# Kernel optimization log

Hardware: AMD Instinct MI355X
Metric: run time of the kernel (lower is better)

Reference implementation:

```python
import jax, jax.numpy as jnp
import numpy as np

B, S, E, NH = 2, 1024, 2048, 16
DH = E // NH
EPS = 1e-6

def setup_inputs() -> dict:
    key = jax.random.key(0)
    ks = jax.random.split(key, 6)
    q = jax.random.normal(ks[0], (B, S, E), dtype=jnp.float32)
    k = jax.random.normal(ks[1], (B, S, E), dtype=jnp.float32)
    v = jax.random.normal(ks[2], (B, S, E), dtype=jnp.float32)
    Wi = jax.random.normal(ks[3], (3 * E, NH), dtype=jnp.float32) * 0.02
    bi = jax.random.normal(ks[4], (NH,), dtype=jnp.float32) * 0.1
    Wf = jax.random.normal(ks[5], (3 * E, NH), dtype=jnp.float32) * 0.02
    bf = jnp.linspace(3.0, 6.0, NH, dtype=jnp.float32)  # bias_linspace_initializer(3,6)
    ln_scale = jnp.ones((E,), dtype=jnp.float32)
    return {"q": q, "k": k, "v": v, "Wi": Wi, "bi": bi, "Wf": Wf, "bf": bf, "ln_scale": ln_scale}

def _mlstm_forward(q, k, v, Wi, bi, Wf, bf, ln_scale):
    b, s, e = q.shape
    nh = Wi.shape[1]
    dh = e // nh
    x = jnp.concatenate([q, k, v], axis=-1)                     # (B,S,3E)
    ig = (x @ Wi + bi).transpose(0, 2, 1)[..., None]            # (B,NH,S,1)
    fg = (x @ Wf + bf).transpose(0, 2, 1)[..., None]            # (B,NH,S,1)
    split = lambda t: t.reshape(b, s, nh, dh).transpose(0, 2, 1, 3)
    qh, kh, vh = split(q), split(k), split(v)                   # (B,NH,S,DH)
    # parallel_stabilized_simple backend
    log_f = jax.nn.log_sigmoid(fg)                              # (B,NH,S,1)
    log_f_cum = jnp.concatenate(
        [jnp.zeros((b, nh, 1, 1), q.dtype), jnp.cumsum(log_f, axis=2)], axis=2
    )                                                           # (B,NH,S+1,1)
    # D[i,j] = cumsum[i] - cumsum[j] on causal part
    fg_mat = log_f_cum - jnp.transpose(log_f_cum, (0, 1, 3, 2)) # (B,NH,S+1,S+1)
    ltr = jnp.tril(jnp.ones((s, s), dtype=bool))
    log_fg = jnp.where(ltr, fg_mat[:, :, 1:, 1:], -jnp.inf)     # (B,NH,S,S)
    log_D = log_fg + jnp.transpose(ig, (0, 1, 3, 2))            # + i_j per column
    max_log_D = jnp.max(log_D, axis=-1, keepdims=True)          # (B,NH,S,1)
    D = jnp.exp(log_D - max_log_D)
    qk = jnp.einsum('bhsd,bhtd->bhst', qh, kh) / jnp.sqrt(jnp.asarray(dh, q.dtype))
    C = qk * D                                                  # (B,NH,S,S)
    normalizer = jnp.maximum(jnp.abs(C.sum(-1, keepdims=True)), jnp.exp(-max_log_D))
    Cn = C / (normalizer + EPS)
    h = jnp.einsum('bhst,bhtd->bhsd', Cn, vh)                   # (B,NH,S,DH)
    # MultiHeadLayerNorm: normalize over DH per head, scale (no bias)
    mu = h.mean(-1, keepdims=True)
    var = ((h - mu) ** 2).mean(-1, keepdims=True)
    hn = (h - mu) * jax.lax.rsqrt(var + EPS)
    hn = hn * ln_scale.reshape(1, nh, 1, dh)
    return hn.transpose(0, 2, 1, 3).reshape(b, s, e)            # (B,S,E)

def reference(q, k, v, Wi, bi, Wf, bf, ln_scale):
    return _mlstm_forward(q, k, v, Wi, bi, Wf, bf, ln_scale)
```

## Files before the change

kernel.cpp:

```cpp
#include <hip/hip_runtime.h>
#include <hip/hip_bf16.h>

#define B_   2
#define S_   1024
#define E_   2048
#define NH_  16
#define DH_  128
#define EPS_ 1e-6f

using half8   = __attribute__((ext_vector_type(8))) _Float16;
using floatx4 = __attribute__((ext_vector_type(4))) float;

__device__ __forceinline__ half8 cvt8h(const float* __restrict__ p) {
    float4 a = *(const float4*)p;
    float4 b = *(const float4*)(p + 4);
    half8 r;
    r[0] = (_Float16)a.x; r[1] = (_Float16)a.y;
    r[2] = (_Float16)a.z; r[3] = (_Float16)a.w;
    r[4] = (_Float16)b.x; r[5] = (_Float16)b.y;
    r[6] = (_Float16)b.z; r[7] = (_Float16)b.w;
    return r;
}

__global__ __launch_bounds__(256, 4) void gates_kernel(
    const float* __restrict__ q, const float* __restrict__ k,
    const float* __restrict__ v, const float* __restrict__ Wi,
    const float* __restrict__ Wf, float* __restrict__ pre_i,
    float* __restrict__ pre_f, _Float16* __restrict__ qhg,
    _Float16* __restrict__ khg, _Float16* __restrict__ vtg)
{
    __shared__ __attribute__((aligned(16))) _Float16 xs[32 * 264];
    __shared__ __attribute__((aligned(16))) _Float16 wt[32 * 264];

    const int t    = threadIdx.x;
    const int w    = t >> 6, lane = t & 63, quad = lane >> 4, l15 = lane & 15;
    const int mw   = w & 1, nw = w >> 1;
    const int m0   = blockIdx.x * 32;
    const int by   = blockIdx.y;
    const int kbase = by * 768;
    const int bblk = m0 >> 10;
    const int s0   = m0 & 1023;

    floatx4 acc = {0.f, 0.f, 0.f, 0.f};

    for (int c = 0; c < 3; ++c) {
        __syncthreads();
        const int e0   = kbase + c * 256;
        const int tsel = e0 >> 11;
        const int el0  = e0 & 2047;
        const float* xb = (tsel == 0) ? q : (tsel == 1) ? k : v;
        _Float16* fout = (tsel == 0) ? qhg : khg;
        #pragma unroll
        for (int i = 0; i < 4; ++i) {
            int g = t + i * 256;
            int row = g >> 5, grp = g & 31;
            half8 s8 = cvt8h(xb + (size_t)(m0 + row) * E_ + el0 + grp * 8);
            *(half8*)(&xs[row * 264 + grp * 8]) = s8;
            if (tsel < 2) {
                int el = el0 + grp * 8;
                int h  = el >> 7, d = el & 127;
                *(half8*)(fout + ((size_t)(bblk * NH_ + h) * S_ + s0 + row) * DH_ + d) = s8;
            }
        }
        {
            const int kk = t;
            const float* wiRow = Wi + (size_t)(e0 + kk) * NH_;
            const float* wfRow = Wf + (size_t)(e0 + kk) * NH_;
            float wif[16], wff[16];
            #pragma unroll
            for (int i4 = 0; i4 < 4; ++i4) {
                float4 a = *(const float4*)(wiRow + i4 * 4);
                wif[i4*4+0]=a.x; wif[i4*4+1]=a.y; wif[i4*4+2]=a.z; wif[i4*4+3]=a.w;
                float4 b = *(const float4*)(wfRow + i4 * 4);
                wff[i4*4+0]=b.x; wff[i4*4+1]=b.y; wff[i4*4+2]=b.z; wff[i4*4+3]=b.w;
            }
            #pragma unroll
            for (int hh = 0; hh < 16; ++hh) wt[hh * 264 + kk]        = (_Float16)wif[hh];
            #pragma unroll
            for (int hh = 0; hh < 16; ++hh) wt[(16 + hh) * 264 + kk] = (_Float16)wff[hh];
        }
        __syncthreads();
        if (tsel == 2) {
            const int col = t;
            const int el  = el0 + col;
            const int h   = el >> 7, d = el & 127;
            _Float16 tmp[32];
            #pragma unroll
            for (int r = 0; r < 32; ++r) tmp[r] = xs[r * 264 + col];
            const size_t vo = ((size_t)(bblk * NH_ + h) * DH_ + d) * S_ + s0;
            #pragma unroll
            for (int i = 0; i < 4; ++i)
                *(half8*)(vtg + vo + i * 8) = *(half8*)(&tmp[i * 8]);
        }
        #pragma unroll
        for (int ks = 0; ks < 8; ++ks) {
            half8 af = *(const half8*)(&xs[(mw * 16 + l15) * 264 + ks * 32 + quad * 8]);
            half8 bw = *(const half8*)(&wt[(nw * 16 + l15) * 264 + ks * 32 + quad * 8]);
            acc = __builtin_amdgcn_mfma_f32_16x16x32_f16(af, bw, acc, 0, 0, 0);
        }
    }
    #pragma unroll
    for (int reg = 0; reg < 4; ++reg) {
        int m   = m0 + mw * 16 + quad * 4 + reg;
        int b   = m >> 10, s = m & 1023;
        int col = nw * 16 + l15;
        float vacc = acc[reg];
        if (col < 16)
            pre_i[((size_t)(by * 32 + b * NH_ + col)) * S_ + s] = vacc;
        else
            pre_f[((size_t)(by * 32 + b * NH_ + col - 16)) * S_ + s] = vacc;
    }
}

__global__ __launch_bounds__(1024, 1) void scan_kernel(
    const float* __restrict__ pre_i, const float* __restrict__ pre_f,
    float* __restrict__ Aj, float* __restrict__ Cq,
    float* __restrict__ NFo, const float* __restrict__ bi,
    const float* __restrict__ bfb)
{
    __shared__ float wsumF[16], wmaxA[16];
    const int bh   = blockIdx.x;
    const int h    = bh & 15;
    const int t    = threadIdx.x;
    const int lane = t & 63, wv = t >> 6;

    float igv = bi[h], x = bfb[h];
    #pragma unroll
    for (int y = 0; y < 8; ++y) {
        igv += pre_i[((size_t)(y * 32 + bh)) * S_ + t];
        x   += pre_f[((size_t)(y * 32 + bh)) * S_ + t];
    }
    float lfv = (x >= 0.f) ? -log1pf(__expf(-x)) : (x - log1pf(__expf(x)));

    float sc = lfv;
    #pragma unroll
    for (int off = 1; off < 64; off <<= 1) {
        float o = __shfl_up(sc, off);
        if (lane >= off) sc += o;
    }
    if (lane == 63) wsumF[wv] = sc;
    __syncthreads();
    float Foff = 0.f;
    for (int i = 0; i < wv; ++i) Foff += wsumF[i];
    float F = Foff + sc;
    float a = igv - F;

    float ms = a;
    #pragma unroll
    for (int off = 1; off < 64; off <<= 1) {
        float o = __shfl_up(ms, off);
        if (lane >= off) ms = fmaxf(ms, o);
    }
    if (lane == 63) wmaxA[wv] = ms;
    __syncthreads();
    float Moff = -3.0e38f;
    for (int i = 0; i < wv; ++i) Moff = fmaxf(Moff, wmaxA[i]);
    float M = fmaxf(Moff, ms);

    size_t o = (size_t)bh * S_ + t;
    Aj[o]  = a;
    Cq[o]  = -M;
    NFo[o] = expf(fminf(-(F + M), 80.f));
}

__global__ __launch_bounds__(256, 2) void attn_kernel(
    const _Float16* __restrict__ qh, const _Float16* __restrict__ kh,
    const _Float16* __restrict__ vtg, const float* __restrict__ Aj,
    const float* __restrict__ Cq, const float* __restrict__ NFi,
    const float* __restrict__ lnsc, float* __restrict__ out)
{
    __shared__ __attribute__((aligned(16))) _Float16 Ks[64 * 136];
    __shared__ __attribute__((aligned(16))) _Float16 Vt[128 * 72];
    __shared__ __attribute__((aligned(16))) _Float16 Pb[64 * 72];
    __shared__ float aj[64];

    const int t    = threadIdx.x;
    const int w    = t >> 6, lane = t & 63, quad = lane >> 4, l15 = lane & 15;
    const int L    = blockIdx.x;
    int qi, bh;
    if (L < 256) { qi = L >> 5;                bh = L & 31; }
    else         { qi = 15 - ((L - 256) >> 5); bh = (L - 256) & 31; }
    const int b    = bh >> 4, h = bh & 15;
    const int q0   = qi * 64;
    const int krow = t >> 2, kd0 = (t & 3) * 32;
    const int vd   = t >> 1, vj0 = (t & 1) * 32;

    float ci_r[4], nfv_r[4];
    #pragma unroll
    for (int reg = 0; reg < 4; ++reg) {
        int rl = w * 16 + quad * 4 + reg;
        ci_r[reg]  = Cq[(size_t)bh * S_ + q0 + rl];
        nfv_r[reg] = NFi[(size_t)bh * S_ + q0 + rl];
    }
    half8 aq[4];
    {
        const _Float16* qrow = qh + ((size_t)bh * S_ + q0 + w * 16 + l15) * DH_;
        #pragma unroll
        for (int ks = 0; ks < 4; ++ks)
            aq[ks] = *(const half8*)(qrow + ks * 32 + quad * 8);
    }

    half8 kreg[4], vreg[4];
    float ajreg = 0.f;
    {
        const _Float16* kp = kh + ((size_t)bh * S_ + krow) * DH_ + kd0;
        const _Float16* vp = vtg + ((size_t)bh * DH_ + vd) * S_ + vj0;
        #pragma unroll
        for (int i = 0; i < 4; ++i) { kreg[i] = *(const half8*)(kp + i * 8);
                                      vreg[i] = *(const half8*)(vp + i * 8); }
    }
    if (t < 64) ajreg = Aj[(size_t)bh * S_ + t];

    #pragma unroll
    for (int i = 0; i < 4; ++i) {
        *(half8*)(&Ks[krow * 136 + kd0 + i * 8]) = kreg[i];
        *(half8*)(&Vt[vd * 72 + vj0 + i * 8])    = vreg[i];
    }
    if (t < 64) aj[t] = ajreg;
    __syncthreads();

    floatx4 acc_h[8];
    #pragma unroll
    for (int i = 0; i < 8; ++i) acc_h[i] = (floatx4){0.f, 0.f, 0.f, 0.f};
    float lrun[4] = {0.f, 0.f, 0.f, 0.f};
    const float rscale = 0.08838834764831845f;

    for (int kt = 0; kt <= qi; ++kt) {
        if (kt < qi) {
            const int j0n = (kt + 1) * 64;
            const _Float16* kp = kh + ((size_t)bh * S_ + j0n + krow) * DH_ + kd0;
            const _Float16* vp = vtg + ((size_t)bh * DH_ + vd) * S_ + j0n + vj0;
            #pragma unroll
            for (int i = 0; i < 4; ++i) { kreg[i] = *(const half8*)(kp + i * 8);
                                          vreg[i] = *(const half8*)(vp + i * 8); }
            if (t < 64) ajreg = Aj[(size_t)bh * S_ + j0n + t];
        }

        floatx4 sacc[4];
        #pragma unroll
        for (int nt = 0; nt < 4; ++nt) sacc[nt] = (floatx4){0.f, 0.f, 0.f, 0.f};
        #pragma unroll
        for (int ks = 0; ks < 4; ++ks) {
            #pragma unroll
            for (int nt = 0; nt < 4; ++nt) {
                half8 bk = *(const half8*)(&Ks[(nt * 16 + l15) * 136 + ks * 32 + quad * 8]);
                sacc[nt] = __builtin_amdgcn_mfma_f32_16x16x32_f16(aq[ks], bk, sacc[nt], 0, 0, 0);
            }
        }
        const bool diag = (kt == qi);
        #pragma unroll
        for (int nt = 0; nt < 4; ++nt) {
            int jl = nt * 16 + l15;
            float a_j = aj[jl];
            #pragma unroll
            for (int reg = 0; reg < 4; ++reg) {
                int rl = w * 16 + quad * 4 + reg;
                float p = 0.f;
                if (!diag || (jl <= rl))
                    p = sacc[nt][reg] * rscale * __expf(fminf(ci_r[reg] + a_j, 0.f));
                lrun[reg] += p;
                Pb[rl * 72 + jl] = (_Float16)p;
            }
        }
        #pragma unroll
        for (int ks2 = 0; ks2 < 2; ++ks2) {
            half8 ap = *(const half8*)(&Pb[(w * 16 + l15) * 72 + ks2 * 32 + quad * 8]);
            #pragma unroll
            for (int nt2 = 0; nt2 < 8; ++nt2) {
                half8 bv = *(const half8*)(&Vt[(nt2 * 16 + l15) * 72 + ks2 * 32 + quad * 8]);
                acc_h[nt2] = __builtin_amdgcn_mfma_f32_16x16x32_f16(ap, bv, acc_h[nt2], 0, 0, 0);
            }
        }

        __syncthreads();
        if (kt < qi) {
            #pragma unroll
            for (int i = 0; i < 4; ++i) {
                *(half8*)(&Ks[krow * 136 + kd0 + i * 8]) = kreg[i];
                *(half8*)(&Vt[vd * 72 + vj0 + i * 8])    = vreg[i];
            }
            if (t < 64) aj[t] = ajreg;
            __syncthreads();
        }
    }

    #pragma unroll
    for (int reg = 0; reg < 4; ++reg) {
        float l = lrun[reg];
        #pragma unroll
        for (int off = 1; off < 16; off <<= 1) l += __shfl_xor(l, off);
        int rl = w * 16 + quad * 4 + reg;
        float nrm = fmaxf(fabsf(l), nfv_r[reg]) + EPS_;
        float inv = 1.f / nrm;
        float hv[8];
        float sum = 0.f, sq = 0.f;
        #pragma unroll
        for (int nt2 = 0; nt2 < 8; ++nt2) {
            float x = acc_h[nt2][reg] * inv;
            hv[nt2] = x; sum += x; sq += x * x;
        }
        #pragma unroll
        for (int off = 1; off < 16; off <<= 1) {
            sum += __shfl_xor(sum, off);
            sq  += __shfl_xor(sq, off);
        }
        float mean = sum * (1.f / 128.f);
        float var  = fmaxf(sq * (1.f / 128.f) - mean * mean, 0.f);
        float rstd = rsqrtf(var + EPS_);
        size_t orow = ((size_t)b * S_ + q0 + rl) * E_ + h * DH_;
        #pragma unroll
        for (int nt2 = 0; nt2 < 8; ++nt2) {
            int d = nt2 * 16 + l15;
            out[orow + d] = (hv[nt2] - mean) * rstd * lnsc[h * DH_ + d];
        }
    }
}

extern "C" void kernel_launch(void* const* d_in, const int* in_sizes, int n_in,
                              void* d_out, int out_size, void* d_ws, size_t ws_size,
                              hipStream_t stream)
{
    const float* q    = (const float*)d_in[0];
    const float* k    = (const float*)d_in[1];
    const float* v    = (const float*)d_in[2];
    const float* Wi   = (const float*)d_in[3];
    const float* bi   = (const float*)d_in[4];
    const float* Wf   = (const float*)d_in[5];
    const float* bfb  = (const float*)d_in[6];
    const float* lnsc = (const float*)d_in[7];
    float* out        = (float*)d_out;

    const int NS  = B_ * NH_ * S_;
    float* pre_i = (float*)d_ws;
    float* pre_f = pre_i + 8 * NS;
    float* Aj    = pre_f + 8 * NS;
    float* Cq    = Aj + NS;
    float* NFa   = Cq + NS;
    _Float16* qh  = (_Float16*)(NFa + NS);
    _Float16* kh  = qh + (size_t)32 * S_ * DH_;
    _Float16* vtg = kh + (size_t)32 * S_ * DH_;

    gates_kernel<<<dim3(64, 8), 256, 0, stream>>>(q, k, v, Wi, Wf, pre_i, pre_f,
                                                  qh, kh, vtg);
    scan_kernel<<<dim3(32), 1024, 0, stream>>>(pre_i, pre_f, Aj, Cq, NFa, bi, bfb);
    attn_kernel<<<dim3(512), 256, 0, stream>>>(qh, kh, vtg, Aj, Cq, NFa, lnsc, out);
}
```

Measured before the change: 149.1 us.

## Pair complementary query tiles per block to balance causal work and share K/V tiles

Each block now handles two 64-row query tiles, qpi and 15-qpi. Waves 0-1 take the short tile and waves 2-3 the long one, with each wave computing 32 rows across two MFMA row-subtiles. K/V tiles are loaded once per block and reused by both query tiles, which gives every block the same causal work and halves the grid to 256 blocks. The cost is more registers per wave (launch bounds drop to one block per SM) and lower occupancy, and waves on the short tile sit idle through the later iterations while still hitting the barriers.

```diff
diff --git a/kernel.cpp b/kernel.cpp
--- a/kernel.cpp
+++ b/kernel.cpp
@@ -163,7 +163,7 @@
     NFo[o] = expf(fminf(-(F + M), 80.f));
 }
 
-__global__ __launch_bounds__(256, 2) void attn_kernel(
+__global__ __launch_bounds__(256, 1) void attn_kernel(
     const _Float16* __restrict__ qh, const _Float16* __restrict__ kh,
     const _Float16* __restrict__ vtg, const float* __restrict__ Aj,
     const float* __restrict__ Cq, const float* __restrict__ NFi,
@@ -171,33 +171,38 @@
 {
     __shared__ __attribute__((aligned(16))) _Float16 Ks[64 * 136];
     __shared__ __attribute__((aligned(16))) _Float16 Vt[128 * 72];
-    __shared__ __attribute__((aligned(16))) _Float16 Pb[64 * 72];
+    __shared__ __attribute__((aligned(16))) _Float16 Pb[128 * 72];
     __shared__ float aj[64];
 
     const int t    = threadIdx.x;
     const int w    = t >> 6, lane = t & 63, quad = lane >> 4, l15 = lane & 15;
-    const int L    = blockIdx.x;
-    int qi, bh;
-    if (L < 256) { qi = L >> 5;                bh = L & 31; }
-    else         { qi = 15 - ((L - 256) >> 5); bh = (L - 256) & 31; }
+    const int bid  = blockIdx.x;
+    const int bh   = bid & 31;
+    const int qpi  = bid >> 5;
     const int b    = bh >> 4, h = bh & 15;
-    const int q0   = qi * 64;
+    const int myq  = (w < 2) ? qpi : (15 - qpi);
+    const int ktN  = 15 - qpi;
+    const int qrow0 = myq * 64 + (w & 1) * 32;
+    const int prow0 = w * 32;
     const int krow = t >> 2, kd0 = (t & 3) * 32;
     const int vd   = t >> 1, vj0 = (t & 1) * 32;
 
-    float ci_r[4], nfv_r[4];
-    #pragma unroll
-    for (int reg = 0; reg < 4; ++reg) {
-        int rl = w * 16 + quad * 4 + reg;
-        ci_r[reg]  = Cq[(size_t)bh * S_ + q0 + rl];
-        nfv_r[reg] = NFi[(size_t)bh * S_ + q0 + rl];
-    }
-    half8 aq[4];
-    {
-        const _Float16* qrow = qh + ((size_t)bh * S_ + q0 + w * 16 + l15) * DH_;
+    float ci_r[2][4], nfv_r[2][4];
+    #pragma unroll
+    for (int s = 0; s < 2; ++s)
+        #pragma unroll
+        for (int reg = 0; reg < 4; ++reg) {
+            int rl = qrow0 + s * 16 + quad * 4 + reg;
+            ci_r[s][reg]  = Cq[(size_t)bh * S_ + rl];
+            nfv_r[s][reg] = NFi[(size_t)bh * S_ + rl];
+        }
+    half8 aq[2][4];
+    #pragma unroll
+    for (int s = 0; s < 2; ++s) {
+        const _Float16* qrow = qh + ((size_t)bh * S_ + qrow0 + s * 16 + l15) * DH_;
         #pragma unroll
         for (int ks = 0; ks < 4; ++ks)
-            aq[ks] = *(const half8*)(qrow + ks * 32 + quad * 8);
+            aq[s][ks] = *(const half8*)(qrow + ks * 32 + quad * 8);
     }
 
     half8 kreg[4], vreg[4];
@@ -219,14 +224,16 @@
     if (t < 64) aj[t] = ajreg;
     __syncthreads();
 
-    floatx4 acc_h[8];
-    #pragma unroll
-    for (int i = 0; i < 8; ++i) acc_h[i] = (floatx4){0.f, 0.f, 0.f, 0.f};
-    float lrun[4] = {0.f, 0.f, 0.f, 0.f};
+    floatx4 acc_h[2][8];
+    #pragma unroll
+    for (int s = 0; s < 2; ++s)
+        #pragma unroll
+        for (int i = 0; i < 8; ++i) acc_h[s][i] = (floatx4){0.f, 0.f, 0.f, 0.f};
+    float lrun[2][4] = {{0.f, 0.f, 0.f, 0.f}, {0.f, 0.f, 0.f, 0.f}};
     const float rscale = 0.08838834764831845f;
 
-    for (int kt = 0; kt <= qi; ++kt) {
-        if (kt < qi) {
+    for (int kt = 0; kt <= ktN; ++kt) {
+        if (kt < ktN) {
             const int j0n = (kt + 1) * 64;
             const _Float16* kp = kh + ((size_t)bh * S_ + j0n + krow) * DH_ + kd0;
             const _Float16* vp = vtg + ((size_t)bh * DH_ + vd) * S_ + j0n + vj0;
@@ -236,44 +243,54 @@
             if (t < 64) ajreg = Aj[(size_t)bh * S_ + j0n + t];
         }
 
-        floatx4 sacc[4];
-        #pragma unroll
-        for (int nt = 0; nt < 4; ++nt) sacc[nt] = (floatx4){0.f, 0.f, 0.f, 0.f};
-        #pragma unroll
-        for (int ks = 0; ks < 4; ++ks) {
+        if (kt <= myq) {
+            floatx4 sacc[2][4];
+            #pragma unroll
+            for (int s = 0; s < 2; ++s)
+                #pragma unroll
+                for (int nt = 0; nt < 4; ++nt) sacc[s][nt] = (floatx4){0.f, 0.f, 0.f, 0.f};
+            #pragma unroll
+            for (int ks = 0; ks < 4; ++ks) {
+                #pragma unroll
+                for (int nt = 0; nt < 4; ++nt) {
+                    half8 bk = *(const half8*)(&Ks[(nt * 16 + l15) * 136 + ks * 32 + quad * 8]);
+                    sacc[0][nt] = __builtin_amdgcn_mfma_f32_16x16x32_f16(aq[0][ks], bk, sacc[0][nt], 0, 0, 0);
+                    sacc[1][nt] = __builtin_amdgcn_mfma_f32_16x16x32_f16(aq[1][ks], bk, sacc[1][nt], 0, 0, 0);
+                }
+            }
+            const bool diag = (kt == myq);
             #pragma unroll
             for (int nt = 0; nt < 4; ++nt) {
-                half8 bk = *(const half8*)(&Ks[(nt * 16 + l15) * 136 + ks * 32 + quad * 8]);
-                sacc[nt] = __builtin_amdgcn_mfma_f32_16x16x32_f16(aq[ks], bk, sacc[nt], 0, 0, 0);
-            }
-        }
-        const bool diag = (kt == qi);
-        #pragma unroll
-        for (int nt = 0; nt < 4; ++nt) {
-            int jl = nt * 16 + l15;
-            float a_j = aj[jl];
-            #pragma unroll
-            for (int reg = 0; reg < 4; ++reg) {
-                int rl = w * 16 + quad * 4 + reg;
-                float p = 0.f;
-                if (!diag || (jl <= rl))
-                    p = sacc[nt][reg] * rscale * __expf(fminf(ci_r[reg] + a_j, 0.f));
-                lrun[reg] += p;
-                Pb[rl * 72 + jl] = (_Float16)p;
-            }
-        }
-        #pragma unroll
-        for (int ks2 = 0; ks2 < 2; ++ks2) {
-            half8 ap = *(const half8*)(&Pb[(w * 16 + l15) * 72 + ks2 * 32 + quad * 8]);
-            #pragma unroll
-            for (int nt2 = 0; nt2 < 8; ++nt2) {
-                half8 bv = *(const half8*)(&Vt[(nt2 * 16 + l15) * 72 + ks2 * 32 + quad * 8]);
-                acc_h[nt2] = __builtin_amdgcn_mfma_f32_16x16x32_f16(ap, bv, acc_h[nt2], 0, 0, 0);
+                int jl = nt * 16 + l15;
+                float a_j = aj[jl];
+                #pragma unroll
+                for (int s = 0; s < 2; ++s) {
+                    #pragma unroll
+                    for (int reg = 0; reg < 4; ++reg) {
+                        int rloc = (w & 1) * 32 + s * 16 + quad * 4 + reg;
+                        float p = 0.f;
+                        if (!diag || (jl <= rloc))
+                            p = sacc[s][nt][reg] * rscale * __expf(fminf(ci_r[s][reg] + a_j, 0.f));
+                        lrun[s][reg] += p;
+                        Pb[(prow0 + s * 16 + quad * 4 + reg) * 72 + jl] = (_Float16)p;
+                    }
+                }
+            }
+            #pragma unroll
+            for (int ks2 = 0; ks2 < 2; ++ks2) {
+                half8 ap0 = *(const half8*)(&Pb[(prow0 + l15) * 72 + ks2 * 32 + quad * 8]);
+                half8 ap1 = *(const half8*)(&Pb[(prow0 + 16 + l15) * 72 + ks2 * 32 + quad * 8]);
+                #pragma unroll
+                for (int nt2 = 0; nt2 < 8; ++nt2) {
+                    half8 bv = *(const half8*)(&Vt[(nt2 * 16 + l15) * 72 + ks2 * 32 + quad * 8]);
+                    acc_h[0][nt2] = __builtin_amdgcn_mfma_f32_16x16x32_f16(ap0, bv, acc_h[0][nt2], 0, 0, 0);
+                    acc_h[1][nt2] = __builtin_amdgcn_mfma_f32_16x16x32_f16(ap1, bv, acc_h[1][nt2], 0, 0, 0);
+                }
             }
         }
 
         __syncthreads();
-        if (kt < qi) {
+        if (kt < ktN) {
             #pragma unroll
             for (int i = 0; i < 4; ++i) {
                 *(half8*)(&Ks[krow * 136 + kd0 + i * 8]) = kreg[i];
@@ -285,33 +302,36 @@
     }
 
     #pragma unroll
-    for (int reg = 0; reg < 4; ++reg) {
-        float l = lrun[reg];
-        #pragma unroll
-        for (int off = 1; off < 16; off <<= 1) l += __shfl_xor(l, off);
-        int rl = w * 16 + quad * 4 + reg;
-        float nrm = fmaxf(fabsf(l), nfv_r[reg]) + EPS_;
-        float inv = 1.f / nrm;
-        float hv[8];
-        float sum = 0.f, sq = 0.f;
-        #pragma unroll
-        for (int nt2 = 0; nt2 < 8; ++nt2) {
-            float x = acc_h[nt2][reg] * inv;
-            hv[nt2] = x; sum += x; sq += x * x;
-        }
-        #pragma unroll
-        for (int off = 1; off < 16; off <<= 1) {
-            sum += __shfl_xor(sum, off);
-            sq  += __shfl_xor(sq, off);
-        }
-        float mean = sum * (1.f / 128.f);
-        float var  = fmaxf(sq * (1.f / 128.f) - mean * mean, 0.f);
-        float rstd = rsqrtf(var + EPS_);
-        size_t orow = ((size_t)b * S_ + q0 + rl) * E_ + h * DH_;
-        #pragma unroll
-        for (int nt2 = 0; nt2 < 8; ++nt2) {
-            int d = nt2 * 16 + l15;
-            out[orow + d] = (hv[nt2] - mean) * rstd * lnsc[h * DH_ + d];
+    for (int s = 0; s < 2; ++s) {
+        #pragma unroll
+        for (int reg = 0; reg < 4; ++reg) {
+            float l = lrun[s][reg];
+            #pragma unroll
+            for (int off = 1; off < 16; off <<= 1) l += __shfl_xor(l, off);
+            int rl = qrow0 + s * 16 + quad * 4 + reg;
+            float nrm = fmaxf(fabsf(l), nfv_r[s][reg]) + EPS_;
+            float inv = 1.f / nrm;
+            float hv[8];
+            float sum = 0.f, sq = 0.f;
+            #pragma unroll
+            for (int nt2 = 0; nt2 < 8; ++nt2) {
+                float x = acc_h[s][nt2][reg] * inv;
+                hv[nt2] = x; sum += x; sq += x * x;
+            }
+            #pragma unroll
+            for (int off = 1; off < 16; off <<= 1) {
+                sum += __shfl_xor(sum, off);
+                sq  += __shfl_xor(sq, off);
+            }
+            float mean = sum * (1.f / 128.f);
+            float var  = fmaxf(sq * (1.f / 128.f) - mean * mean, 0.f);
+            float rstd = rsqrtf(var + EPS_);
+            size_t orow = ((size_t)b * S_ + rl) * E_ + h * DH_;
+            #pragma unroll
+            for (int nt2 = 0; nt2 < 8; ++nt2) {
+                int d = nt2 * 16 + l15;
+                out[orow + d] = (hv[nt2] - mean) * rstd * lnsc[h * DH_ + d];
+            }
         }
     }
 }
@@ -343,5 +363,5 @@
     gates_kernel<<<dim3(64, 8), 256, 0, stream>>>(q, k, v, Wi, Wf, pre_i, pre_f,
                                                   qh, kh, vtg);
     scan_kernel<<<dim3(32), 1024, 0, stream>>>(pre_i, pre_f, Aj, Cq, NFa, bi, bfb);
-    attn_kernel<<<dim3(512), 256, 0, stream>>>(qh, kh, vtg, Aj, Cq, NFa, lnsc, out);
-}
+    attn_kernel<<<dim3(256), 256, 0, stream>>>(qh, kh, vtg, Aj, Cq, NFa, lnsc, out);
+}
```

Result: slower. 162.8 us (+9.2%).
